# Kernel tuning notes

Hardware: AMD Instinct MI355X
Metric: run time of the kernel (lower is better)

The kernel has to match this reference:

```python
import jax, jax.numpy as jnp
import numpy as np

N = 50000
E = 640000
D_IN = 128
HID = 128
N_CLASSES = 40
N_LAYERS = 2
BN_EPS = 1e-5


def setup_inputs() -> dict:
    key = jax.random.key(0)
    ks = jax.random.split(key, 16)
    s_in = 1.0 / np.sqrt(D_IN)
    s_h = 1.0 / np.sqrt(HID)
    inp = {
        "x": jax.random.normal(ks[0], (N, D_IN), dtype=jnp.float32),
        "edge_index": jax.random.randint(ks[1], (2, E), 0, N, dtype=jnp.int64),
        # fcs[0]: Linear(in, hid)
        "fc0_w": jax.random.uniform(ks[2], (HID, D_IN), jnp.float32, -s_in, s_in),
        "fc0_b": jax.random.uniform(ks[3], (HID,), jnp.float32, -s_in, s_in),
        # BatchNorm params: bns[0..num_layers]
        "bn_scale": jnp.ones((N_LAYERS + 1, HID), jnp.float32),
        "bn_bias": jnp.zeros((N_LAYERS + 1, HID), jnp.float32),
        # SAGEConv per layer: lin_l (applied to aggregated neighbors), lin_r (root), bias=False
        "lin_l": jax.random.uniform(ks[4], (N_LAYERS, HID, HID), jnp.float32, -s_h, s_h),
        "lin_r": jax.random.uniform(ks[5], (N_LAYERS, HID, HID), jnp.float32, -s_h, s_h),
        # shared W: Linear(hid, hid)
        "W_w": jax.random.uniform(ks[6], (HID, HID), jnp.float32, -s_h, s_h),
        "W_b": jax.random.uniform(ks[7], (HID,), jnp.float32, -s_h, s_h),
        # out_lin: Linear(hid, num_classes)
        "out_w": jax.random.uniform(ks[8], (N_CLASSES, HID), jnp.float32, -s_h, s_h),
        "out_b": jax.random.uniform(ks[9], (N_CLASSES,), jnp.float32, -s_h, s_h),
    }
    return inp


def _batch_norm(h, scale, bias):
    # training-mode BN over the node dimension (biased variance, as in torch)
    mu = jnp.mean(h, axis=0)
    var = jnp.mean(jnp.square(h - mu), axis=0)
    return (h - mu) * jax.lax.rsqrt(var + BN_EPS) * scale + bias


def reference(x, edge_index, fc0_w, fc0_b, bn_scale, bn_bias, lin_l, lin_r, W_w, W_b, out_w, out_b):
    src, dst = edge_index[0], edge_index[1]  # messages flow src(j) -> dst(i)
    n = x.shape[0]
    deg = jax.ops.segment_sum(jnp.ones((src.shape[0],), x.dtype), dst, num_segments=n)
    inv_deg = (1.0 / jnp.maximum(deg, 1.0))[:, None]  # [N,1]

    h = x @ fc0_w.T + fc0_b
    h = _batch_norm(h, bn_scale[0], bn_bias[0])
    h = jax.nn.relu(h)  # dropout p=0 / eval -> identity

    for i in range(N_LAYERS):
        # SAGEConv: mean-aggregate neighbor features, then lin_l(agg) + lin_r(root)
        agg = jax.ops.segment_sum(h[src], dst, num_segments=n) * inv_deg  # [N,HID]
        h = agg @ lin_l[i].T + h @ lin_r[i].T
        h = h @ W_w.T + W_b
        h = _batch_norm(h, bn_scale[i + 1], bn_bias[i + 1])
        h = jax.nn.relu(h)

    return h @ out_w.T + out_b
```

## Files before the change

### kernel.cpp

```cpp
#include <hip/hip_runtime.h>
#include <hip/hip_bf16.h>

#define NN 50000
#define EE 640000
#define HD 128
#define NCLS 40
#define BN_EPS 1e-5f
#define GTILES 1563
#define GGRID 782
#define NB 98
#define ECHUNK 5000

typedef short bf16x8 __attribute__((ext_vector_type(8)));
typedef float f32x4 __attribute__((ext_vector_type(4)));

__device__ __forceinline__ short f2bf(float f) {
    __hip_bfloat16 h = __float2bfloat16(f);
    return *reinterpret_cast<short*>(&h);
}
__device__ __forceinline__ float bflo(unsigned int v) { return __uint_as_float(v << 16); }
__device__ __forceinline__ float bfhi(unsigned int v) { return __uint_as_float(v & 0xffff0000u); }
__device__ __forceinline__ unsigned int packbf(float a, float b) {
    return (unsigned)(unsigned short)f2bf(a) | ((unsigned)(unsigned short)f2bf(b) << 16);
}

__global__ void detect_kernel(const void* __restrict__ ei, int* __restrict__ flag) {
    int t = threadIdx.x;
    const long long* p = (const long long*)ei;
    long long v = p[(size_t)t * (EE / 256)];
    if (v < 0 || v >= NN) atomicOr(flag, 1);
}

__global__ __launch_bounds__(512) void hist_kernel(const void* __restrict__ ei,
                                                   const int* __restrict__ flag,
                                                   int* __restrict__ cnt) {
    __shared__ int lh[NB];
    int t = threadIdx.x, b = blockIdx.x;
    if (t < NB) lh[t] = 0;
    __syncthreads();
    bool narrow = (*flag != 0);
    int e0 = b * ECHUNK;
    for (int e = e0 + t; e < e0 + ECHUNK; e += 512) {
        int d = narrow ? ((const int*)ei)[EE + e] : (int)((const long long*)ei)[EE + e];
        atomicAdd(&lh[d >> 9], 1);
    }
    __syncthreads();
    if (t < NB) cnt[b * NB + t] = lh[t];
}

__global__ void bucket_off2(const int* __restrict__ cnt, int* __restrict__ boffs,
                            int* __restrict__ ebase) {
    __shared__ int s[128];
    int k = threadIdx.x;
    int tot = 0;
    if (k < NB)
        for (int b = 0; b < 128; ++b) tot += cnt[b * NB + k];
    s[k] = tot;
    __syncthreads();
    for (int o = 1; o < 128; o <<= 1) {
        int u = (k >= o) ? s[k - o] : 0;
        __syncthreads();
        s[k] += u;
        __syncthreads();
    }
    if (k < NB) {
        int base = s[k] - tot;
        ebase[k] = base;
        if (k == NB - 1) ebase[NB] = base + tot;
        int run = base;
        for (int b = 0; b < 128; ++b) {
            boffs[b * NB + k] = run;
            run += cnt[b * NB + k];
        }
    }
}

__global__ __launch_bounds__(512) void bucket_scatter(const void* __restrict__ ei,
                                                      const int* __restrict__ flag,
                                                      const int* __restrict__ boffs,
                                                      uint2* __restrict__ bkt) {
    __shared__ int lc[NB];
    int t = threadIdx.x, b = blockIdx.x;
    if (t < NB) lc[t] = boffs[b * NB + t];
    __syncthreads();
    bool narrow = (*flag != 0);
    int e0 = b * ECHUNK;
    for (int e = e0 + t; e < e0 + ECHUNK; e += 512) {
        int s, d;
        if (narrow) {
            s = ((const int*)ei)[e];
            d = ((const int*)ei)[EE + e];
        } else {
            s = (int)((const long long*)ei)[e];
            d = (int)((const long long*)ei)[EE + e];
        }
        int pos = atomicAdd(&lc[d >> 9], 1);
        bkt[pos] = make_uint2((unsigned)s, (unsigned)d);
    }
}

__global__ __launch_bounds__(512) void bucket_build(const uint2* __restrict__ bkt,
                                                    const int* __restrict__ ebase,
                                                    int* __restrict__ rowptr,
                                                    float* __restrict__ invdeg,
                                                    int* __restrict__ adj) {
    __shared__ int ldeg[512];
    __shared__ int lcur[512];
    __shared__ int ladj[8192];
    int t = threadIdx.x, k = blockIdx.x;
    int nodeBase = k << 9;
    int nn = NN - nodeBase;
    if (nn > 512) nn = 512;
    int e0 = ebase[k], e1 = ebase[k + 1];
    int ne = e1 - e0;
    ldeg[t] = 0;
    __syncthreads();
    for (int i = e0 + t; i < e1; i += 512)
        atomicAdd(&ldeg[(int)bkt[i].y - nodeBase], 1);
    __syncthreads();
    int d = ldeg[t];
    lcur[t] = d;
    __syncthreads();
    for (int o = 1; o < 512; o <<= 1) {
        int u = (t >= o) ? lcur[t - o] : 0;
        __syncthreads();
        lcur[t] += u;
        __syncthreads();
    }
    int excl = lcur[t] - d;
    if (t < nn) {
        rowptr[nodeBase + t] = e0 + excl;
        invdeg[nodeBase + t] = 1.0f / (float)(d > 1 ? d : 1);
    }
    if (k == 0 && t == 0) rowptr[NN] = EE;
    __syncthreads();
    lcur[t] = excl;
    __syncthreads();
    if (ne <= 8192) {
        for (int i = e0 + t; i < e1; i += 512) {
            uint2 p = bkt[i];
            int pos = atomicAdd(&lcur[(int)p.y - nodeBase], 1);
            ladj[pos] = (int)p.x;
        }
        __syncthreads();
        for (int i = t; i < ne; i += 512) adj[e0 + i] = ladj[i];
    } else {
        for (int i = e0 + t; i < e1; i += 512) {
            uint2 p = bkt[i];
            int pos = atomicAdd(&lcur[(int)p.y - nodeBase], 1);
            adj[e0 + pos] = (int)p.x;
        }
    }
}

__global__ void combine_w(const float* __restrict__ Ww, const float* __restrict__ linl,
                          const float* __restrict__ linr, ushort* __restrict__ Wcb) {
    int k = threadIdx.x;
    int m = blockIdx.x;
    int which = blockIdx.y;
    const float* lin = ((which & 1) ? linr : linl) + (which >> 1) * HD * HD;
    __shared__ float wrow[HD];
    wrow[k] = Ww[m * HD + k];
    __syncthreads();
    float acc = 0.f;
    for (int j = 0; j < HD; ++j) acc += wrow[j] * lin[j * HD + k];
    Wcb[which * HD * HD + m * HD + k] = (unsigned short)f2bf(acc);
}

__global__ void convw_kernel(const float* __restrict__ W, ushort* __restrict__ Wb) {
    int i = blockIdx.x * 256 + threadIdx.x;
    if (i < HD * HD) Wb[i] = (unsigned short)f2bf(W[i]);
}

__global__ void convw48(const float* __restrict__ W, ushort* __restrict__ Wb) {
    int i = blockIdx.x * 256 + threadIdx.x;
    if (i < 48 * HD) Wb[i] = (i < NCLS * HD) ? (unsigned short)f2bf(W[i]) : (unsigned short)0;
}

template <bool DUAL, bool F32A>
__global__ __launch_bounds__(256) void gemm_mfma(const void* __restrict__ A1v,
                                                 const ushort* __restrict__ A2g,
                                                 const float* __restrict__ bnp,
                                                 const ushort* __restrict__ W1,
                                                 const ushort* __restrict__ W2,
                                                 ushort* __restrict__ Y,
                                                 float* __restrict__ parts) {
    __shared__ __align__(16) char lds[32768];
    const int t = threadIdx.x;
    const int l = t & 63, w = t >> 6;
    const int lr = l & 15, lg = l >> 4;
    constexpr int BUFSZ = DUAL ? 16384 : 8192;

    bf16x8 bw1[2][4], bw2[2][4];
    {
        const uint4* srcw = (const uint4*)W1;
        for (int i = t; i < 2048; i += 256) ((uint4*)lds)[i] = srcw[i];
        __syncthreads();
#pragma unroll
        for (int cc = 0; cc < 2; ++cc)
#pragma unroll
            for (int kk = 0; kk < 4; ++kk)
                bw1[cc][kk] = *(const bf16x8*)&lds[((w * 2 + cc) * 16 + lr) * 256 + kk * 64 + lg * 16];
        if constexpr (DUAL) {
            __syncthreads();
            const uint4* srcw2 = (const uint4*)W2;
            for (int i = t; i < 2048; i += 256) ((uint4*)lds)[i] = srcw2[i];
            __syncthreads();
#pragma unroll
            for (int cc = 0; cc < 2; ++cc)
#pragma unroll
                for (int kk = 0; kk < 4; ++kk)
                    bw2[cc][kk] = *(const bf16x8*)&lds[((w * 2 + cc) * 16 + lr) * 256 + kk * 64 + lg * 16];
        }
        __syncthreads();
    }

    const int t0 = blockIdx.x;
    const int t1 = blockIdx.x + GGRID;
    const bool has2 = (t1 < GTILES);

    f32x4 ss[2] = {}, sq[2] = {};

    uint4 st1[2], st2[2], fx[4];
    auto stage_load = [&](int tile) {
#pragma unroll
        for (int s = 0; s < 2; ++s) {
            int o = s * 4096 + t * 16;
            int po = o ^ (((o >> 8) & 7) << 4);
            int grow = tile * 32 + (po >> 8);
            if (grow > NN - 1) grow = NN - 1;
            if constexpr (F32A) {
                const char* src = (const char*)A1v + (size_t)grow * 512 + (size_t)(po & 255) * 2;
                fx[s * 2] = *(const uint4*)src;
                fx[s * 2 + 1] = *(const uint4*)(src + 16);
            } else {
                st1[s] = *(const uint4*)((const char*)A1v + (size_t)grow * 256 + (po & 255));
            }
            if constexpr (DUAL)
                st2[s] = *(const uint4*)((const char*)A2g + (size_t)grow * 256 + (po & 255));
        }
    };
    auto stage_write = [&](int buf) {
        char* base = lds + buf * BUFSZ;
#pragma unroll
        for (int s = 0; s < 2; ++s) {
            int o = s * 4096 + t * 16;
            uint4 v;
            if constexpr (F32A) {
                uint4 a = fx[s * 2], b2 = fx[s * 2 + 1];
                v.x = packbf(__uint_as_float(a.x), __uint_as_float(a.y));
                v.y = packbf(__uint_as_float(a.z), __uint_as_float(a.w));
                v.z = packbf(__uint_as_float(b2.x), __uint_as_float(b2.y));
                v.w = packbf(__uint_as_float(b2.z), __uint_as_float(b2.w));
            } else {
                v = st1[s];
            }
            *(uint4*)(base + o) = v;
            if constexpr (DUAL) {
                int po = o ^ (((o >> 8) & 7) << 4);
                int col0 = (po & 255) >> 1;
                float4 sa = *(const float4*)&bnp[col0];
                float4 sb = *(const float4*)&bnp[col0 + 4];
                float4 ba = *(const float4*)&bnp[HD + col0];
                float4 bb2 = *(const float4*)&bnp[HD + col0 + 4];
                uint4 h;
                h.x = packbf(fmaxf(bflo(st2[s].x) * sa.x + ba.x, 0.f),
                             fmaxf(bfhi(st2[s].x) * sa.y + ba.y, 0.f));
                h.y = packbf(fmaxf(bflo(st2[s].y) * sa.z + ba.z, 0.f),
                             fmaxf(bfhi(st2[s].y) * sa.w + ba.w, 0.f));
                h.z = packbf(fmaxf(bflo(st2[s].z) * sb.x + bb2.x, 0.f),
                             fmaxf(bfhi(st2[s].z) * sb.y + bb2.y, 0.f));
                h.w = packbf(fmaxf(bflo(st2[s].w) * sb.z + bb2.z, 0.f),
                             fmaxf(bfhi(st2[s].w) * sb.w + bb2.w, 0.f));
                *(uint4*)(base + 8192 + o) = h;
            }
        }
    };
    auto compute = [&](int tile, int buf) {
        const char* base = lds + buf * BUFSZ;
        f32x4 acc[2][2] = {};
#pragma unroll
        for (int rf = 0; rf < 2; ++rf) {
            int rowb = (rf * 16 + lr) * 256;
            int sw = (lr & 7) << 4;
            bf16x8 a1[4], a2[4];
#pragma unroll
            for (int kk = 0; kk < 4; ++kk) {
                int q = rowb + ((kk * 64 + lg * 16) ^ sw);
                a1[kk] = *(const bf16x8*)(base + q);
                if constexpr (DUAL) a2[kk] = *(const bf16x8*)(base + 8192 + q);
            }
#pragma unroll
            for (int kk = 0; kk < 4; ++kk)
#pragma unroll
                for (int cc = 0; cc < 2; ++cc) {
                    acc[rf][cc] = __builtin_amdgcn_mfma_f32_16x16x32_bf16(bw1[cc][kk], a1[kk], acc[rf][cc], 0, 0, 0);
                    if constexpr (DUAL)
                        acc[rf][cc] = __builtin_amdgcn_mfma_f32_16x16x32_bf16(bw2[cc][kk], a2[kk], acc[rf][cc], 0, 0, 0);
                }
        }
#pragma unroll
        for (int rf = 0; rf < 2; ++rf) {
            int row = tile * 32 + rf * 16 + lr;
            if (row < NN) {
#pragma unroll
                for (int cc = 0; cc < 2; ++cc) {
                    f32x4 v = acc[rf][cc];
                    uint2 o;
                    o.x = packbf(v[0], v[1]);
                    o.y = packbf(v[2], v[3]);
                    *(uint2*)&Y[(size_t)row * HD + (w * 2 + cc) * 16 + lg * 4] = o;
                    ss[cc] += v;
                    sq[cc] += v * v;
                }
            }
        }
    };

    stage_load(t0);
    stage_write(0);
    if (has2) stage_load(t1);
    __syncthreads();
    compute(t0, 0);
    if (has2) {
        stage_write(1);
        __syncthreads();
        compute(t1, 1);
    }

#pragma unroll
    for (int cc = 0; cc < 2; ++cc)
#pragma unroll
        for (int j = 0; j < 4; ++j) {
            float a = ss[cc][j], b = sq[cc][j];
#pragma unroll
            for (int m = 1; m < 16; m <<= 1) {
                a += __shfl_xor(a, m);
                b += __shfl_xor(b, m);
            }
            if (lr == 0) {
                int col = (w * 2 + cc) * 16 + lg * 4 + j;
                parts[(size_t)col * GGRID + blockIdx.x] = a;
                parts[(size_t)(HD + col) * GGRID + blockIdx.x] = b;
            }
        }
}

__global__ __launch_bounds__(256) void bn_fold2(const float* __restrict__ parts,
                                                const float* __restrict__ scale,
                                                const float* __restrict__ bias,
                                                float* __restrict__ bnp) {
    __shared__ float r1[256], r2[256];
    int j = blockIdx.x;
    int t = threadIdx.x;
    float a = 0.f, b = 0.f;
    for (int i = t; i < GGRID; i += 256) {
        a += parts[(size_t)j * GGRID + i];
        b += parts[(size_t)(HD + j) * GGRID + i];
    }
    r1[t] = a; r2[t] = b;
    __syncthreads();
    for (int o = 128; o; o >>= 1) {
        if (t < o) { r1[t] += r1[t + o]; r2[t] += r2[t + o]; }
        __syncthreads();
    }
    if (t == 0) {
        float mu = r1[0] * (1.0f / NN);
        float var = r2[0] * (1.0f / NN) - mu * mu;
        float sc = scale[j] * rsqrtf(var + BN_EPS);
        bnp[j] = sc;
        bnp[HD + j] = bias[j] - mu * sc;
    }
}

__global__ __launch_bounds__(256) void agg_kernel(const ushort* __restrict__ Hp,
                                                  const float* __restrict__ bnp,
                                                  const int* __restrict__ adj,
                                                  const int* __restrict__ rowptr,
                                                  const float* __restrict__ invdeg,
                                                  ushort* __restrict__ A) {
    int node = blockIdx.x * 4 + (threadIdx.x >> 6);
    if (node >= NN) return;
    int l = threadIdx.x & 63;
    int slot = l >> 4, col = l & 15;
    float sc[8], bi[8];
    {
        float4 a = *(const float4*)&bnp[col * 8];
        float4 b = *(const float4*)&bnp[col * 8 + 4];
        float4 c = *(const float4*)&bnp[HD + col * 8];
        float4 d = *(const float4*)&bnp[HD + col * 8 + 4];
        sc[0] = a.x; sc[1] = a.y; sc[2] = a.z; sc[3] = a.w;
        sc[4] = b.x; sc[5] = b.y; sc[6] = b.z; sc[7] = b.w;
        bi[0] = c.x; bi[1] = c.y; bi[2] = c.z; bi[3] = c.w;
        bi[4] = d.x; bi[5] = d.y; bi[6] = d.z; bi[7] = d.w;
    }
    int b = rowptr[node], e = rowptr[node + 1];
    float id = invdeg[node];
    float acc[8] = {};
    for (int i = b; i < e; i += 8) {
        int i0 = i + slot, i1 = i + 4 + slot;
        bool v0 = i0 < e, v1 = i1 < e;
        int s0 = adj[v0 ? i0 : i];
        int s1 = adj[v1 ? i1 : i];
        uint4 a = *(const uint4*)&Hp[(size_t)s0 * HD + col * 8];
        uint4 c = *(const uint4*)&Hp[(size_t)s1 * HD + col * 8];
        float m0 = v0 ? 1.f : 0.f, m1 = v1 ? 1.f : 0.f;
        acc[0] += fmaxf(bflo(a.x) * sc[0] + bi[0], 0.f) * m0 + fmaxf(bflo(c.x) * sc[0] + bi[0], 0.f) * m1;
        acc[1] += fmaxf(bfhi(a.x) * sc[1] + bi[1], 0.f) * m0 + fmaxf(bfhi(c.x) * sc[1] + bi[1], 0.f) * m1;
        acc[2] += fmaxf(bflo(a.y) * sc[2] + bi[2], 0.f) * m0 + fmaxf(bflo(c.y) * sc[2] + bi[2], 0.f) * m1;
        acc[3] += fmaxf(bfhi(a.y) * sc[3] + bi[3], 0.f) * m0 + fmaxf(bfhi(c.y) * sc[3] + bi[3], 0.f) * m1;
        acc[4] += fmaxf(bflo(a.z) * sc[4] + bi[4], 0.f) * m0 + fmaxf(bflo(c.z) * sc[4] + bi[4], 0.f) * m1;
        acc[5] += fmaxf(bfhi(a.z) * sc[5] + bi[5], 0.f) * m0 + fmaxf(bfhi(c.z) * sc[5] + bi[5], 0.f) * m1;
        acc[6] += fmaxf(bflo(a.w) * sc[6] + bi[6], 0.f) * m0 + fmaxf(bflo(c.w) * sc[6] + bi[6], 0.f) * m1;
        acc[7] += fmaxf(bfhi(a.w) * sc[7] + bi[7], 0.f) * m0 + fmaxf(bfhi(c.w) * sc[7] + bi[7], 0.f) * m1;
    }
#pragma unroll
    for (int c2 = 0; c2 < 8; ++c2) {
        acc[c2] += __shfl_xor(acc[c2], 16);
        acc[c2] += __shfl_xor(acc[c2], 32);
    }
    if (slot == 0) {
        uint4 o;
        o.x = packbf(acc[0] * id, acc[1] * id);
        o.y = packbf(acc[2] * id, acc[3] * id);
        o.z = packbf(acc[4] * id, acc[5] * id);
        o.w = packbf(acc[6] * id, acc[7] * id);
        *(uint4*)&A[(size_t)node * HD + col * 8] = o;
    }
}

__global__ __launch_bounds__(256) void out_mfma(const ushort* __restrict__ Hp,
                                                const float* __restrict__ bnp,
                                                const ushort* __restrict__ W48,
                                                const float* __restrict__ B,
                                                float* __restrict__ out) {
    __shared__ __align__(16) char lds[16384];
    __shared__ float blds[48];
    const int t = threadIdx.x;
    const int l = t & 63;
    const int lr = l & 15, lg = l >> 4;
    if (t < 48) blds[t] = (t < NCLS) ? B[t] : 0.f;

    bf16x8 bw[3][4];
#pragma unroll
    for (int cc = 0; cc < 3; ++cc)
#pragma unroll
        for (int kk = 0; kk < 4; ++kk)
            bw[cc][kk] = *(const bf16x8*)&W48[(size_t)(cc * 16 + lr) * HD + kk * 32 + lg * 8];

    const int t0 = blockIdx.x, t1 = blockIdx.x + GGRID;
    const bool has2 = (t1 < GTILES);

    uint4 s1a[2];
    auto stage_load = [&](int tile) {
#pragma unroll
        for (int s = 0; s < 2; ++s) {
            int o = s * 4096 + t * 16;
            int po = o ^ (((o >> 8) & 7) << 4);
            int grow = tile * 32 + (po >> 8);
            if (grow > NN - 1) grow = NN - 1;
            s1a[s] = *(const uint4*)((const char*)Hp + (size_t)grow * 256 + (po & 255));
        }
    };
    auto stage_write = [&](int buf) {
        char* base = lds + buf * 8192;
#pragma unroll
        for (int s = 0; s < 2; ++s) {
            int o = s * 4096 + t * 16;
            int po = o ^ (((o >> 8) & 7) << 4);
            int col0 = (po & 255) >> 1;
            float4 sa = *(const float4*)&bnp[col0];
            float4 sb = *(const float4*)&bnp[col0 + 4];
            float4 ba = *(const float4*)&bnp[HD + col0];
            float4 bb2 = *(const float4*)&bnp[HD + col0 + 4];
            uint4 h;
            h.x = packbf(fmaxf(bflo(s1a[s].x) * sa.x + ba.x, 0.f),
                         fmaxf(bfhi(s1a[s].x) * sa.y + ba.y, 0.f));
            h.y = packbf(fmaxf(bflo(s1a[s].y) * sa.z + ba.z, 0.f),
                         fmaxf(bfhi(s1a[s].y) * sa.w + ba.w, 0.f));
            h.z = packbf(fmaxf(bflo(s1a[s].z) * sb.x + bb2.x, 0.f),
                         fmaxf(bfhi(s1a[s].z) * sb.y + bb2.y, 0.f));
            h.w = packbf(fmaxf(bflo(s1a[s].w) * sb.z + bb2.z, 0.f),
                         fmaxf(bfhi(s1a[s].w) * sb.w + bb2.w, 0.f));
            *(uint4*)(base + o) = h;
        }
    };
    auto compute = [&](int tile, int buf) {
        const char* base = lds + buf * 8192;
        f32x4 acc[2][3] = {};
#pragma unroll
        for (int rf = 0; rf < 2; ++rf) {
            int rowb = (rf * 16 + lr) * 256;
            int sw = (lr & 7) << 4;
            bf16x8 a1[4];
#pragma unroll
            for (int kk = 0; kk < 4; ++kk)
                a1[kk] = *(const bf16x8*)(base + rowb + ((kk * 64 + lg * 16) ^ sw));
#pragma unroll
            for (int kk = 0; kk < 4; ++kk)
#pragma unroll
                for (int cc = 0; cc < 3; ++cc)
                    acc[rf][cc] = __builtin_amdgcn_mfma_f32_16x16x32_bf16(bw[cc][kk], a1[kk], acc[rf][cc], 0, 0, 0);
        }
#pragma unroll
        for (int rf = 0; rf < 2; ++rf) {
            int row = tile * 32 + rf * 16 + lr;
            if (row < NN) {
#pragma unroll
                for (int cc = 0; cc < 3; ++cc) {
                    int col = cc * 16 + lg * 4;
                    if (col < NCLS) {
                        float4 bv = *(const float4*)&blds[col];
                        float2 lo = {acc[rf][cc][0] + bv.x, acc[rf][cc][1] + bv.y};
                        float2 hi = {acc[rf][cc][2] + bv.z, acc[rf][cc][3] + bv.w};
                        *(float2*)&out[(size_t)row * NCLS + col] = lo;
                        *(float2*)&out[(size_t)row * NCLS + col + 2] = hi;
                    }
                }
            }
        }
    };

    stage_load(t0);
    stage_write(0);
    if (has2) stage_load(t1);
    __syncthreads();
    compute(t0, 0);
    if (has2) {
        stage_write(1);
        __syncthreads();
        compute(t1, 1);
    }
}

extern "C" void kernel_launch(void* const* d_in, const int* in_sizes, int n_in,
                              void* d_out, int out_size, void* d_ws, size_t ws_size,
                              hipStream_t stream) {
    const float* x = (const float*)d_in[0];
    const void* ei = d_in[1];
    const float* fc0_w = (const float*)d_in[2];
    const float* bn_scale = (const float*)d_in[4];
    const float* bn_bias = (const float*)d_in[5];
    const float* lin_l = (const float*)d_in[6];
    const float* lin_r = (const float*)d_in[7];
    const float* W_w = (const float*)d_in[8];
    const float* out_w = (const float*)d_in[10];
    const float* out_b = (const float*)d_in[11];
    float* out = (float*)d_out;

    char* p = (char*)d_ws;
    auto alloc = [&](size_t bytes) -> void* {
        void* r = (void*)p;
        p += (bytes + 255) & ~(size_t)255;
        return r;
    };
    int* eflag = (int*)alloc(256);
    size_t ctrl_bytes = (size_t)(p - (char*)d_ws);
    int* rowptr = (int*)alloc((NN + 1) * 4);
    float* invdeg = (float*)alloc(NN * 4);
    int* adj = (int*)alloc(EE * 4);
    int* cnt = (int*)alloc(128 * NB * 4);
    int* boffs = (int*)alloc(128 * NB * 4);
    int* ebase = (int*)alloc((NB + 1) * 4);
    uint2* bkt = (uint2*)alloc((size_t)EE * 8);
    float* parts = (float*)alloc((size_t)256 * GGRID * 4);
    float* bnp = (float*)alloc(3 * 256 * 4);
    ushort* Wcb = (ushort*)alloc(4 * HD * HD * 2);
    ushort* wfc0 = (ushort*)alloc(HD * HD * 2);
    ushort* wo48 = (ushort*)alloc(48 * HD * 2);
    ushort* hpreA = (ushort*)alloc((size_t)NN * HD * 2);
    ushort* hpreB = (ushort*)alloc((size_t)NN * HD * 2);
    ushort* aggb = (ushort*)alloc((size_t)NN * HD * 2);

    hipMemsetAsync(d_ws, 0, ctrl_bytes, stream);

    detect_kernel<<<1, 256, 0, stream>>>(ei, eflag);
    hist_kernel<<<128, 512, 0, stream>>>(ei, eflag, cnt);
    bucket_off2<<<1, 128, 0, stream>>>(cnt, boffs, ebase);
    bucket_scatter<<<128, 512, 0, stream>>>(ei, eflag, boffs, bkt);
    bucket_build<<<NB, 512, 0, stream>>>(bkt, ebase, rowptr, invdeg, adj);

    combine_w<<<dim3(HD, 4), HD, 0, stream>>>(W_w, lin_l, lin_r, Wcb);
    convw_kernel<<<64, 256, 0, stream>>>(fc0_w, wfc0);
    convw48<<<24, 256, 0, stream>>>(out_w, wo48);

    gemm_mfma<false, true><<<GGRID, 256, 0, stream>>>(x, nullptr, nullptr, wfc0, nullptr, hpreA, parts);
    bn_fold2<<<128, 256, 0, stream>>>(parts, bn_scale, bn_bias, bnp);

    ushort* hcur = hpreA;
    ushort* hnext = hpreB;
    for (int layer = 0; layer < 2; ++layer) {
        float* bp = bnp + layer * 256;
        agg_kernel<<<(NN + 3) / 4, 256, 0, stream>>>(hcur, bp, adj, rowptr, invdeg, aggb);
        const ushort* Wl = Wcb + (size_t)(layer * 2 + 0) * HD * HD;
        const ushort* Wr = Wcb + (size_t)(layer * 2 + 1) * HD * HD;
        gemm_mfma<true, false><<<GGRID, 256, 0, stream>>>(aggb, hcur, bp, Wl, Wr, hnext, parts);
        bn_fold2<<<128, 256, 0, stream>>>(parts, bn_scale + (layer + 1) * HD,
                                          bn_bias + (layer + 1) * HD, bnp + (layer + 1) * 256);
        ushort* tmp = hcur; hcur = hnext; hnext = tmp;
    }

    out_mfma<<<GGRID, 256, 0, stream>>>(hcur, bnp + 2 * 256, wo48, out_b, out);
}
```

Baseline: 181.1 us.

## Fuse neighbor aggregation into the SAGE layer GEMM and pack bucket entries

Each layer now runs one kernel per 32-node tile. It gathers the neighbor mean straight into LDS, applies BN+ReLU to the root rows, and runs the dual MFMA GEMM, so the aggregated bf16 tensor no longer makes a round trip through global memory and one launch per layer is dropped. The bucket sort also packs (local dst, src) into a single 32-bit word, halving that buffer's traffic. In exchange, each block carries its weight registers while doing the latency-bound gather and has no tile pipelining. Occupancy may fall, and the gather's parallelism is tied to 4 warps of 8 nodes each.

```diff
diff --git a/kernel.cpp b/kernel.cpp
--- a/kernel.cpp
+++ b/kernel.cpp
@@ -78,7 +78,7 @@
 __global__ __launch_bounds__(512) void bucket_scatter(const void* __restrict__ ei,
                                                       const int* __restrict__ flag,
                                                       const int* __restrict__ boffs,
-                                                      uint2* __restrict__ bkt) {
+                                                      unsigned int* __restrict__ bkt) {
     __shared__ int lc[NB];
     int t = threadIdx.x, b = blockIdx.x;
     if (t < NB) lc[t] = boffs[b * NB + t];
@@ -95,11 +95,11 @@
             d = (int)((const long long*)ei)[EE + e];
         }
         int pos = atomicAdd(&lc[d >> 9], 1);
-        bkt[pos] = make_uint2((unsigned)s, (unsigned)d);
-    }
-}
-
-__global__ __launch_bounds__(512) void bucket_build(const uint2* __restrict__ bkt,
+        bkt[pos] = ((unsigned)(d & 511) << 17) | (unsigned)s;
+    }
+}
+
+__global__ __launch_bounds__(512) void bucket_build(const unsigned int* __restrict__ bkt,
                                                     const int* __restrict__ ebase,
                                                     int* __restrict__ rowptr,
                                                     float* __restrict__ invdeg,
@@ -116,7 +116,7 @@
     ldeg[t] = 0;
     __syncthreads();
     for (int i = e0 + t; i < e1; i += 512)
-        atomicAdd(&ldeg[(int)bkt[i].y - nodeBase], 1);
+        atomicAdd(&ldeg[bkt[i] >> 17], 1);
     __syncthreads();
     int d = ldeg[t];
     lcur[t] = d;
@@ -138,17 +138,17 @@
     __syncthreads();
     if (ne <= 8192) {
         for (int i = e0 + t; i < e1; i += 512) {
-            uint2 p = bkt[i];
-            int pos = atomicAdd(&lcur[(int)p.y - nodeBase], 1);
-            ladj[pos] = (int)p.x;
+            unsigned int p = bkt[i];
+            int pos = atomicAdd(&lcur[p >> 17], 1);
+            ladj[pos] = (int)(p & 0x1FFFFu);
         }
         __syncthreads();
         for (int i = t; i < ne; i += 512) adj[e0 + i] = ladj[i];
     } else {
         for (int i = e0 + t; i < e1; i += 512) {
-            uint2 p = bkt[i];
-            int pos = atomicAdd(&lcur[(int)p.y - nodeBase], 1);
-            adj[e0 + pos] = (int)p.x;
+            unsigned int p = bkt[i];
+            int pos = atomicAdd(&lcur[p >> 17], 1);
+            adj[e0 + pos] = (int)(p & 0x1FFFFu);
         }
     }
 }
@@ -177,21 +177,16 @@
     if (i < 48 * HD) Wb[i] = (i < NCLS * HD) ? (unsigned short)f2bf(W[i]) : (unsigned short)0;
 }
 
-template <bool DUAL, bool F32A>
-__global__ __launch_bounds__(256) void gemm_mfma(const void* __restrict__ A1v,
-                                                 const ushort* __restrict__ A2g,
-                                                 const float* __restrict__ bnp,
-                                                 const ushort* __restrict__ W1,
-                                                 const ushort* __restrict__ W2,
-                                                 ushort* __restrict__ Y,
-                                                 float* __restrict__ parts) {
+__global__ __launch_bounds__(256) void gemm_fc0(const float* __restrict__ X,
+                                                const ushort* __restrict__ W1,
+                                                ushort* __restrict__ Y,
+                                                float* __restrict__ parts) {
     __shared__ __align__(16) char lds[32768];
     const int t = threadIdx.x;
     const int l = t & 63, w = t >> 6;
     const int lr = l & 15, lg = l >> 4;
-    constexpr int BUFSZ = DUAL ? 16384 : 8192;
-
-    bf16x8 bw1[2][4], bw2[2][4];
+
+    bf16x8 bw1[2][4];
     {
         const uint4* srcw = (const uint4*)W1;
         for (int i = t; i < 2048; i += 256) ((uint4*)lds)[i] = srcw[i];
@@ -201,17 +196,6 @@
 #pragma unroll
             for (int kk = 0; kk < 4; ++kk)
                 bw1[cc][kk] = *(const bf16x8*)&lds[((w * 2 + cc) * 16 + lr) * 256 + kk * 64 + lg * 16];
-        if constexpr (DUAL) {
-            __syncthreads();
-            const uint4* srcw2 = (const uint4*)W2;
-            for (int i = t; i < 2048; i += 256) ((uint4*)lds)[i] = srcw2[i];
-            __syncthreads();
-#pragma unroll
-            for (int cc = 0; cc < 2; ++cc)
-#pragma unroll
-                for (int kk = 0; kk < 4; ++kk)
-                    bw2[cc][kk] = *(const bf16x8*)&lds[((w * 2 + cc) * 16 + lr) * 256 + kk * 64 + lg * 16];
-        }
         __syncthreads();
     }
 
@@ -220,8 +204,7 @@
     const bool has2 = (t1 < GTILES);
 
     f32x4 ss[2] = {}, sq[2] = {};
-
-    uint4 st1[2], st2[2], fx[4];
+    uint4 fx[4];
     auto stage_load = [&](int tile) {
 #pragma unroll
         for (int s = 0; s < 2; ++s) {
@@ -229,75 +212,40 @@
             int po = o ^ (((o >> 8) & 7) << 4);
             int grow = tile * 32 + (po >> 8);
             if (grow > NN - 1) grow = NN - 1;
-            if constexpr (F32A) {
-                const char* src = (const char*)A1v + (size_t)grow * 512 + (size_t)(po & 255) * 2;
-                fx[s * 2] = *(const uint4*)src;
-                fx[s * 2 + 1] = *(const uint4*)(src + 16);
-            } else {
-                st1[s] = *(const uint4*)((const char*)A1v + (size_t)grow * 256 + (po & 255));
-            }
-            if constexpr (DUAL)
-                st2[s] = *(const uint4*)((const char*)A2g + (size_t)grow * 256 + (po & 255));
+            const char* src = (const char*)X + (size_t)grow * 512 + (size_t)(po & 255) * 2;
+            fx[s * 2] = *(const uint4*)src;
+            fx[s * 2 + 1] = *(const uint4*)(src + 16);
         }
     };
     auto stage_write = [&](int buf) {
-        char* base = lds + buf * BUFSZ;
+        char* base = lds + buf * 8192;
 #pragma unroll
         for (int s = 0; s < 2; ++s) {
-            int o = s * 4096 + t * 16;
+            uint4 a = fx[s * 2], b2 = fx[s * 2 + 1];
             uint4 v;
-            if constexpr (F32A) {
-                uint4 a = fx[s * 2], b2 = fx[s * 2 + 1];
-                v.x = packbf(__uint_as_float(a.x), __uint_as_float(a.y));
-                v.y = packbf(__uint_as_float(a.z), __uint_as_float(a.w));
-                v.z = packbf(__uint_as_float(b2.x), __uint_as_float(b2.y));
-                v.w = packbf(__uint_as_float(b2.z), __uint_as_float(b2.w));
-            } else {
-                v = st1[s];
-            }
-            *(uint4*)(base + o) = v;
-            if constexpr (DUAL) {
-                int po = o ^ (((o >> 8) & 7) << 4);
-                int col0 = (po & 255) >> 1;
-                float4 sa = *(const float4*)&bnp[col0];
-                float4 sb = *(const float4*)&bnp[col0 + 4];
-                float4 ba = *(const float4*)&bnp[HD + col0];
-                float4 bb2 = *(const float4*)&bnp[HD + col0 + 4];
-                uint4 h;
-                h.x = packbf(fmaxf(bflo(st2[s].x) * sa.x + ba.x, 0.f),
-                             fmaxf(bfhi(st2[s].x) * sa.y + ba.y, 0.f));
-                h.y = packbf(fmaxf(bflo(st2[s].y) * sa.z + ba.z, 0.f),
-                             fmaxf(bfhi(st2[s].y) * sa.w + ba.w, 0.f));
-                h.z = packbf(fmaxf(bflo(st2[s].z) * sb.x + bb2.x, 0.f),
-                             fmaxf(bfhi(st2[s].z) * sb.y + bb2.y, 0.f));
-                h.w = packbf(fmaxf(bflo(st2[s].w) * sb.z + bb2.z, 0.f),
-                             fmaxf(bfhi(st2[s].w) * sb.w + bb2.w, 0.f));
-                *(uint4*)(base + 8192 + o) = h;
-            }
+            v.x = packbf(__uint_as_float(a.x), __uint_as_float(a.y));
+            v.y = packbf(__uint_as_float(a.z), __uint_as_float(a.w));
+            v.z = packbf(__uint_as_float(b2.x), __uint_as_float(b2.y));
+            v.w = packbf(__uint_as_float(b2.z), __uint_as_float(b2.w));
+            *(uint4*)(base + s * 4096 + t * 16) = v;
         }
     };
     auto compute = [&](int tile, int buf) {
-        const char* base = lds + buf * BUFSZ;
+        const char* base = lds + buf * 8192;
         f32x4 acc[2][2] = {};
 #pragma unroll
         for (int rf = 0; rf < 2; ++rf) {
             int rowb = (rf * 16 + lr) * 256;
             int sw = (lr & 7) << 4;
-            bf16x8 a1[4], a2[4];
-#pragma unroll
-            for (int kk = 0; kk < 4; ++kk) {
-                int q = rowb + ((kk * 64 + lg * 16) ^ sw);
-                a1[kk] = *(const bf16x8*)(base + q);
-                if constexpr (DUAL) a2[kk] = *(const bf16x8*)(base + 8192 + q);
-            }
+            bf16x8 a1[4];
 #pragma unroll
             for (int kk = 0; kk < 4; ++kk)
-#pragma unroll
-                for (int cc = 0; cc < 2; ++cc) {
+                a1[kk] = *(const bf16x8*)(base + rowb + ((kk * 64 + lg * 16) ^ sw));
+#pragma unroll
+            for (int kk = 0; kk < 4; ++kk)
+#pragma unroll
+                for (int cc = 0; cc < 2; ++cc)
                     acc[rf][cc] = __builtin_amdgcn_mfma_f32_16x16x32_bf16(bw1[cc][kk], a1[kk], acc[rf][cc], 0, 0, 0);
-                    if constexpr (DUAL)
-                        acc[rf][cc] = __builtin_amdgcn_mfma_f32_16x16x32_bf16(bw2[cc][kk], a2[kk], acc[rf][cc], 0, 0, 0);
-                }
         }
 #pragma unroll
         for (int rf = 0; rf < 2; ++rf) {
@@ -340,48 +288,60 @@
             }
             if (lr == 0) {
                 int col = (w * 2 + cc) * 16 + lg * 4 + j;
-                parts[(size_t)col * GGRID + blockIdx.x] = a;
-                parts[(size_t)(HD + col) * GGRID + blockIdx.x] = b;
-            }
-        }
-}
-
-__global__ __launch_bounds__(256) void bn_fold2(const float* __restrict__ parts,
-                                                const float* __restrict__ scale,
-                                                const float* __restrict__ bias,
-                                                float* __restrict__ bnp) {
-    __shared__ float r1[256], r2[256];
-    int j = blockIdx.x;
-    int t = threadIdx.x;
-    float a = 0.f, b = 0.f;
-    for (int i = t; i < GGRID; i += 256) {
-        a += parts[(size_t)j * GGRID + i];
-        b += parts[(size_t)(HD + j) * GGRID + i];
-    }
-    r1[t] = a; r2[t] = b;
-    __syncthreads();
-    for (int o = 128; o; o >>= 1) {
-        if (t < o) { r1[t] += r1[t + o]; r2[t] += r2[t + o]; }
-        __syncthreads();
-    }
-    if (t == 0) {
-        float mu = r1[0] * (1.0f / NN);
-        float var = r2[0] * (1.0f / NN) - mu * mu;
-        float sc = scale[j] * rsqrtf(var + BN_EPS);
-        bnp[j] = sc;
-        bnp[HD + j] = bias[j] - mu * sc;
-    }
-}
-
-__global__ __launch_bounds__(256) void agg_kernel(const ushort* __restrict__ Hp,
-                                                  const float* __restrict__ bnp,
-                                                  const int* __restrict__ adj,
-                                                  const int* __restrict__ rowptr,
-                                                  const float* __restrict__ invdeg,
-                                                  ushort* __restrict__ A) {
-    int node = blockIdx.x * 4 + (threadIdx.x >> 6);
-    if (node >= NN) return;
-    int l = threadIdx.x & 63;
+                parts[(size_t)col * GTILES + blockIdx.x] = a;
+                parts[(size_t)(HD + col) * GTILES + blockIdx.x] = b;
+            }
+        }
+}
+
+__global__ __launch_bounds__(256) void layer_fused(const ushort* __restrict__ Hp,
+                                                   const float* __restrict__ bnp,
+                                                   const int* __restrict__ adj,
+                                                   const int* __restrict__ rowptr,
+                                                   const float* __restrict__ invdeg,
+                                                   const ushort* __restrict__ W1,
+                                                   const ushort* __restrict__ W2,
+                                                   ushort* __restrict__ Y,
+                                                   float* __restrict__ parts) {
+    __shared__ __align__(16) char lds[32768];
+    const int t = threadIdx.x;
+    const int l = t & 63, w = t >> 6;
+    const int lr = l & 15, lg = l >> 4;
+
+    bf16x8 bw1[2][4], bw2[2][4];
+    {
+        const uint4* srcw = (const uint4*)W1;
+        for (int i = t; i < 2048; i += 256) ((uint4*)lds)[i] = srcw[i];
+        __syncthreads();
+#pragma unroll
+        for (int cc = 0; cc < 2; ++cc)
+#pragma unroll
+            for (int kk = 0; kk < 4; ++kk)
+                bw1[cc][kk] = *(const bf16x8*)&lds[((w * 2 + cc) * 16 + lr) * 256 + kk * 64 + lg * 16];
+        __syncthreads();
+        const uint4* srcw2 = (const uint4*)W2;
+        for (int i = t; i < 2048; i += 256) ((uint4*)lds)[i] = srcw2[i];
+        __syncthreads();
+#pragma unroll
+        for (int cc = 0; cc < 2; ++cc)
+#pragma unroll
+            for (int kk = 0; kk < 4; ++kk)
+                bw2[cc][kk] = *(const bf16x8*)&lds[((w * 2 + cc) * 16 + lr) * 256 + kk * 64 + lg * 16];
+        __syncthreads();
+    }
+
+    const int tile = blockIdx.x;
+
+    uint4 st2[2];
+#pragma unroll
+    for (int s = 0; s < 2; ++s) {
+        int o = s * 4096 + t * 16;
+        int po = o ^ (((o >> 8) & 7) << 4);
+        int grow = tile * 32 + (po >> 8);
+        if (grow > NN - 1) grow = NN - 1;
+        st2[s] = *(const uint4*)((const char*)Hp + (size_t)grow * 256 + (po & 255));
+    }
+
     int slot = l >> 4, col = l & 15;
     float sc[8], bi[8];
     {
@@ -394,38 +354,151 @@
         bi[0] = c.x; bi[1] = c.y; bi[2] = c.z; bi[3] = c.w;
         bi[4] = d.x; bi[5] = d.y; bi[6] = d.z; bi[7] = d.w;
     }
-    int b = rowptr[node], e = rowptr[node + 1];
-    float id = invdeg[node];
-    float acc[8] = {};
-    for (int i = b; i < e; i += 8) {
-        int i0 = i + slot, i1 = i + 4 + slot;
-        bool v0 = i0 < e, v1 = i1 < e;
-        int s0 = adj[v0 ? i0 : i];
-        int s1 = adj[v1 ? i1 : i];
-        uint4 a = *(const uint4*)&Hp[(size_t)s0 * HD + col * 8];
-        uint4 c = *(const uint4*)&Hp[(size_t)s1 * HD + col * 8];
-        float m0 = v0 ? 1.f : 0.f, m1 = v1 ? 1.f : 0.f;
-        acc[0] += fmaxf(bflo(a.x) * sc[0] + bi[0], 0.f) * m0 + fmaxf(bflo(c.x) * sc[0] + bi[0], 0.f) * m1;
-        acc[1] += fmaxf(bfhi(a.x) * sc[1] + bi[1], 0.f) * m0 + fmaxf(bfhi(c.x) * sc[1] + bi[1], 0.f) * m1;
-        acc[2] += fmaxf(bflo(a.y) * sc[2] + bi[2], 0.f) * m0 + fmaxf(bflo(c.y) * sc[2] + bi[2], 0.f) * m1;
-        acc[3] += fmaxf(bfhi(a.y) * sc[3] + bi[3], 0.f) * m0 + fmaxf(bfhi(c.y) * sc[3] + bi[3], 0.f) * m1;
-        acc[4] += fmaxf(bflo(a.z) * sc[4] + bi[4], 0.f) * m0 + fmaxf(bflo(c.z) * sc[4] + bi[4], 0.f) * m1;
-        acc[5] += fmaxf(bfhi(a.z) * sc[5] + bi[5], 0.f) * m0 + fmaxf(bfhi(c.z) * sc[5] + bi[5], 0.f) * m1;
-        acc[6] += fmaxf(bflo(a.w) * sc[6] + bi[6], 0.f) * m0 + fmaxf(bflo(c.w) * sc[6] + bi[6], 0.f) * m1;
-        acc[7] += fmaxf(bfhi(a.w) * sc[7] + bi[7], 0.f) * m0 + fmaxf(bfhi(c.w) * sc[7] + bi[7], 0.f) * m1;
-    }
-#pragma unroll
-    for (int c2 = 0; c2 < 8; ++c2) {
-        acc[c2] += __shfl_xor(acc[c2], 16);
-        acc[c2] += __shfl_xor(acc[c2], 32);
-    }
-    if (slot == 0) {
-        uint4 o;
-        o.x = packbf(acc[0] * id, acc[1] * id);
-        o.y = packbf(acc[2] * id, acc[3] * id);
-        o.z = packbf(acc[4] * id, acc[5] * id);
-        o.w = packbf(acc[6] * id, acc[7] * id);
-        *(uint4*)&A[(size_t)node * HD + col * 8] = o;
+#pragma unroll 1
+    for (int j = 0; j < 8; ++j) {
+        int node = tile * 32 + w * 8 + j;
+        int r = w * 8 + j;
+        int q = r * 256 + ((col * 16) ^ ((r & 7) << 4));
+        if (node < NN) {
+            int b = rowptr[node], e = rowptr[node + 1];
+            float id = invdeg[node];
+            float acc[8] = {};
+            for (int i = b; i < e; i += 8) {
+                int i0 = i + slot, i1 = i + 4 + slot;
+                bool v0 = i0 < e, v1 = i1 < e;
+                int s0 = adj[v0 ? i0 : i];
+                int s1 = adj[v1 ? i1 : i];
+                uint4 a = *(const uint4*)&Hp[(size_t)s0 * HD + col * 8];
+                uint4 c = *(const uint4*)&Hp[(size_t)s1 * HD + col * 8];
+                float m0 = v0 ? 1.f : 0.f, m1 = v1 ? 1.f : 0.f;
+                acc[0] += fmaxf(bflo(a.x) * sc[0] + bi[0], 0.f) * m0 + fmaxf(bflo(c.x) * sc[0] + bi[0], 0.f) * m1;
+                acc[1] += fmaxf(bfhi(a.x) * sc[1] + bi[1], 0.f) * m0 + fmaxf(bfhi(c.x) * sc[1] + bi[1], 0.f) * m1;
+                acc[2] += fmaxf(bflo(a.y) * sc[2] + bi[2], 0.f) * m0 + fmaxf(bflo(c.y) * sc[2] + bi[2], 0.f) * m1;
+                acc[3] += fmaxf(bfhi(a.y) * sc[3] + bi[3], 0.f) * m0 + fmaxf(bfhi(c.y) * sc[3] + bi[3], 0.f) * m1;
+                acc[4] += fmaxf(bflo(a.z) * sc[4] + bi[4], 0.f) * m0 + fmaxf(bflo(c.z) * sc[4] + bi[4], 0.f) * m1;
+                acc[5] += fmaxf(bfhi(a.z) * sc[5] + bi[5], 0.f) * m0 + fmaxf(bfhi(c.z) * sc[5] + bi[5], 0.f) * m1;
+                acc[6] += fmaxf(bflo(a.w) * sc[6] + bi[6], 0.f) * m0 + fmaxf(bflo(c.w) * sc[6] + bi[6], 0.f) * m1;
+                acc[7] += fmaxf(bfhi(a.w) * sc[7] + bi[7], 0.f) * m0 + fmaxf(bfhi(c.w) * sc[7] + bi[7], 0.f) * m1;
+            }
+#pragma unroll
+            for (int c2 = 0; c2 < 8; ++c2) {
+                acc[c2] += __shfl_xor(acc[c2], 16);
+                acc[c2] += __shfl_xor(acc[c2], 32);
+            }
+            if (slot == 0) {
+                uint4 o;
+                o.x = packbf(acc[0] * id, acc[1] * id);
+                o.y = packbf(acc[2] * id, acc[3] * id);
+                o.z = packbf(acc[4] * id, acc[5] * id);
+                o.w = packbf(acc[6] * id, acc[7] * id);
+                *(uint4*)&lds[q] = o;
+            }
+        } else if (slot == 0) {
+            *(uint4*)&lds[q] = make_uint4(0, 0, 0, 0);
+        }
+    }
+
+#pragma unroll
+    for (int s = 0; s < 2; ++s) {
+        int o = s * 4096 + t * 16;
+        int po = o ^ (((o >> 8) & 7) << 4);
+        int col0 = (po & 255) >> 1;
+        float4 sa = *(const float4*)&bnp[col0];
+        float4 sb = *(const float4*)&bnp[col0 + 4];
+        float4 ba = *(const float4*)&bnp[HD + col0];
+        float4 bb2 = *(const float4*)&bnp[HD + col0 + 4];
+        uint4 h;
+        h.x = packbf(fmaxf(bflo(st2[s].x) * sa.x + ba.x, 0.f),
+                     fmaxf(bfhi(st2[s].x) * sa.y + ba.y, 0.f));
+        h.y = packbf(fmaxf(bflo(st2[s].y) * sa.z + ba.z, 0.f),
+                     fmaxf(bfhi(st2[s].y) * sa.w + ba.w, 0.f));
+        h.z = packbf(fmaxf(bflo(st2[s].z) * sb.x + bb2.x, 0.f),
+                     fmaxf(bfhi(st2[s].z) * sb.y + bb2.y, 0.f));
+        h.w = packbf(fmaxf(bflo(st2[s].w) * sb.z + bb2.z, 0.f),
+                     fmaxf(bfhi(st2[s].w) * sb.w + bb2.w, 0.f));
+        *(uint4*)(lds + 8192 + o) = h;
+    }
+    __syncthreads();
+
+    f32x4 ss[2] = {}, sq[2] = {};
+    f32x4 acc[2][2] = {};
+#pragma unroll
+    for (int rf = 0; rf < 2; ++rf) {
+        int rowb = (rf * 16 + lr) * 256;
+        int sw = (lr & 7) << 4;
+        bf16x8 a1[4], a2[4];
+#pragma unroll
+        for (int kk = 0; kk < 4; ++kk) {
+            int q = rowb + ((kk * 64 + lg * 16) ^ sw);
+            a1[kk] = *(const bf16x8*)(lds + q);
+            a2[kk] = *(const bf16x8*)(lds + 8192 + q);
+        }
+#pragma unroll
+        for (int kk = 0; kk < 4; ++kk)
+#pragma unroll
+            for (int cc = 0; cc < 2; ++cc) {
+                acc[rf][cc] = __builtin_amdgcn_mfma_f32_16x16x32_bf16(bw1[cc][kk], a1[kk], acc[rf][cc], 0, 0, 0);
+                acc[rf][cc] = __builtin_amdgcn_mfma_f32_16x16x32_bf16(bw2[cc][kk], a2[kk], acc[rf][cc], 0, 0, 0);
+            }
+    }
+#pragma unroll
+    for (int rf = 0; rf < 2; ++rf) {
+        int row = tile * 32 + rf * 16 + lr;
+        if (row < NN) {
+#pragma unroll
+            for (int cc = 0; cc < 2; ++cc) {
+                f32x4 v = acc[rf][cc];
+                uint2 o;
+                o.x = packbf(v[0], v[1]);
+                o.y = packbf(v[2], v[3]);
+                *(uint2*)&Y[(size_t)row * HD + (w * 2 + cc) * 16 + lg * 4] = o;
+                ss[cc] += v;
+                sq[cc] += v * v;
+            }
+        }
+    }
+#pragma unroll
+    for (int cc = 0; cc < 2; ++cc)
+#pragma unroll
+        for (int j = 0; j < 4; ++j) {
+            float a = ss[cc][j], b = sq[cc][j];
+#pragma unroll
+            for (int m = 1; m < 16; m <<= 1) {
+                a += __shfl_xor(a, m);
+                b += __shfl_xor(b, m);
+            }
+            if (lr == 0) {
+                int cl = (w * 2 + cc) * 16 + lg * 4 + j;
+                parts[(size_t)cl * GTILES + blockIdx.x] = a;
+                parts[(size_t)(HD + cl) * GTILES + blockIdx.x] = b;
+            }
+        }
+}
+
+__global__ __launch_bounds__(256) void bn_fold2(const float* __restrict__ parts, int n,
+                                                const float* __restrict__ scale,
+                                                const float* __restrict__ bias,
+                                                float* __restrict__ bnp) {
+    __shared__ float r1[256], r2[256];
+    int j = blockIdx.x;
+    int t = threadIdx.x;
+    float a = 0.f, b = 0.f;
+    for (int i = t; i < n; i += 256) {
+        a += parts[(size_t)j * GTILES + i];
+        b += parts[(size_t)(HD + j) * GTILES + i];
+    }
+    r1[t] = a; r2[t] = b;
+    __syncthreads();
+    for (int o = 128; o; o >>= 1) {
+        if (t < o) { r1[t] += r1[t + o]; r2[t] += r2[t + o]; }
+        __syncthreads();
+    }
+    if (t == 0) {
+        float mu = r1[0] * (1.0f / NN);
+        float var = r2[0] * (1.0f / NN) - mu * mu;
+        float sc = scale[j] * rsqrtf(var + BN_EPS);
+        bnp[j] = sc;
+        bnp[HD + j] = bias[j] - mu * sc;
     }
 }
 
@@ -562,15 +635,14 @@
     int* cnt = (int*)alloc(128 * NB * 4);
     int* boffs = (int*)alloc(128 * NB * 4);
     int* ebase = (int*)alloc((NB + 1) * 4);
-    uint2* bkt = (uint2*)alloc((size_t)EE * 8);
-    float* parts = (float*)alloc((size_t)256 * GGRID * 4);
+    unsigned int* bkt = (unsigned int*)alloc((size_t)EE * 4);
+    float* parts = (float*)alloc((size_t)256 * GTILES * 4);
     float* bnp = (float*)alloc(3 * 256 * 4);
     ushort* Wcb = (ushort*)alloc(4 * HD * HD * 2);
     ushort* wfc0 = (ushort*)alloc(HD * HD * 2);
     ushort* wo48 = (ushort*)alloc(48 * HD * 2);
     ushort* hpreA = (ushort*)alloc((size_t)NN * HD * 2);
     ushort* hpreB = (ushort*)alloc((size_t)NN * HD * 2);
-    ushort* aggb = (ushort*)alloc((size_t)NN * HD * 2);
 
     hipMemsetAsync(d_ws, 0, ctrl_bytes, stream);
 
@@ -584,18 +656,17 @@
     convw_kernel<<<64, 256, 0, stream>>>(fc0_w, wfc0);
     convw48<<<24, 256, 0, stream>>>(out_w, wo48);
 
-    gemm_mfma<false, true><<<GGRID, 256, 0, stream>>>(x, nullptr, nullptr, wfc0, nullptr, hpreA, parts);
-    bn_fold2<<<128, 256, 0, stream>>>(parts, bn_scale, bn_bias, bnp);
+    gemm_fc0<<<GGRID, 256, 0, stream>>>(x, wfc0, hpreA, parts);
+    bn_fold2<<<128, 256, 0, stream>>>(parts, GGRID, bn_scale, bn_bias, bnp);
 
     ushort* hcur = hpreA;
     ushort* hnext = hpreB;
     for (int layer = 0; layer < 2; ++layer) {
         float* bp = bnp + layer * 256;
-        agg_kernel<<<(NN + 3) / 4, 256, 0, stream>>>(hcur, bp, adj, rowptr, invdeg, aggb);
         const ushort* Wl = Wcb + (size_t)(layer * 2 + 0) * HD * HD;
         const ushort* Wr = Wcb + (size_t)(layer * 2 + 1) * HD * HD;
-        gemm_mfma<true, false><<<GGRID, 256, 0, stream>>>(aggb, hcur, bp, Wl, Wr, hnext, parts);
-        bn_fold2<<<128, 256, 0, stream>>>(parts, bn_scale + (layer + 1) * HD,
+        layer_fused<<<GTILES, 256, 0, stream>>>(hcur, bp, adj, rowptr, invdeg, Wl, Wr, hnext, parts);
+        bn_fold2<<<128, 256, 0, stream>>>(parts, GTILES, bn_scale + (layer + 1) * HD,
                                           bn_bias + (layer + 1) * HD, bnp + (layer + 1) * 256);
         ushort* tmp = hcur; hcur = hnext; hnext = tmp;
     }
```

Measured after the change: 274.5 us. +51.6%, slower.
